# Kernel tuning notes

Hardware: AMD Instinct MI355X
Metric: run time of the kernel (lower is better)

The kernel has to match this reference:

```python
import jax, jax.numpy as jnp
from jax import lax
import numpy as np

TAG_NAMES = ["O", "B-MAT", "I-MAT", "B-PRO", "I-PRO", "B-APL", "I-APL", "B-SMT", "I-SMT", "B-CMT", "I-CMT", "B-DSC", "I-DSC"]
IMP = -100.0


def _init_crf_params(key):
    # torchcrf initializes uniform(-0.1, 0.1); CRF_NEW then clamps invalid
    # BIO transitions to -100 per define_invalid_crf_transitions/init_crf_transitions.
    K = len(TAG_NAMES)
    k1, k2, k3 = jax.random.split(key, 3)
    start = np.array(jax.random.uniform(k1, (K,), minval=-0.1, maxval=0.1), dtype=np.float32)
    end = np.array(jax.random.uniform(k2, (K,), minval=-0.1, maxval=0.1), dtype=np.float32)
    trans = np.array(jax.random.uniform(k3, (K, K), minval=-0.1, maxval=0.1), dtype=np.float32)
    pref = [t[0] for t in TAG_NAMES]
    ent = [t.split('-')[1] if '-' in t else '' for t in TAG_NAMES]
    for i in range(K):
        if pref[i] in ('B', 'I'):  # invalid begin/end for BIO
            start[i] = IMP
            end[i] = IMP
    for i in range(K):
        for j in range(K):
            # invalid_transitions_position: O -> I  (B->P, I->P are empty sets)
            if pref[i] == 'O' and pref[j] == 'I':
                trans[i, j] = IMP
            # invalid_transitions_tags: B->I, I->I across different entity types
            if pref[i] in ('B', 'I') and pref[j] == 'I' and ent[i] != ent[j]:
                trans[i, j] = IMP
    return jnp.asarray(start), jnp.asarray(end), jnp.asarray(trans)


def setup_inputs() -> dict:
    key = jax.random.key(0)
    k_em, k_tag, k_p = jax.random.split(key, 3)
    B, T, K = 4096, 512, len(TAG_NAMES)
    emissions = jax.random.normal(k_em, (B, T, K), dtype=jnp.float32)
    tags = jax.random.randint(k_tag, (B, T), 0, K, dtype=jnp.int64)
    mask = jnp.ones((B, T), dtype=bool)
    start_transitions, end_transitions, transitions = _init_crf_params(k_p)
    return {"emissions": emissions, "tags": tags, "mask": mask,
            "start_transitions": start_transitions,
            "end_transitions": end_transitions,
            "transitions": transitions}


def reference(emissions, tags, mask, start_transitions, end_transitions, transitions):
    # torchcrf CRF.forward with batch_first=True, reduction='sum':
    # returns sum over batch of log p(tags | emissions).
    B, T, K = emissions.shape
    maskf = mask.astype(emissions.dtype)

    # ---- numerator: score of the given tag path ----
    emit = jnp.take_along_axis(emissions, tags[..., None], axis=2)[..., 0]  # [B,T]
    trans = transitions[tags[:, :-1], tags[:, 1:]]                           # [B,T-1]
    num = start_transitions[tags[:, 0]] + emit[:, 0]
    num = num + jnp.sum((trans + emit[:, 1:]) * maskf[:, 1:], axis=1)
    seq_ends = jnp.sum(mask.astype(jnp.int32), axis=1) - 1                   # [B]
    last_tags = tags[jnp.arange(B), seq_ends]
    num = num + end_transitions[last_tags]

    # ---- denominator: log partition via forward-algorithm scan over time ----
    em_t = jnp.swapaxes(emissions, 0, 1)   # [T,B,K]
    mask_t = jnp.swapaxes(mask, 0, 1)      # [T,B]
    score0 = start_transitions + em_t[0]   # [B,K]

    def step(score, xs):
        em, m = xs  # em: [B,K], m: [B]
        # broadcast: [B,K_from,1] + [K_from,K_to] + [B,1,K_to]
        nxt = jax.nn.logsumexp(score[:, :, None] + transitions[None] + em[:, None, :], axis=1)
        return jnp.where(m[:, None], nxt, score), None

    score, _ = lax.scan(step, score0, (em_t[1:], mask_t[1:]))
    denom = jax.nn.logsumexp(score + end_transitions, axis=1)  # [B]

    return jnp.sum(num - denom)
```

## Files before the change

kernel.cpp:

```cpp
#include <hip/hip_runtime.h>


typedef float f4 __attribute__((ext_vector_type(4)));
typedef short s4 __attribute__((ext_vector_type(4)));
typedef int   i2 __attribute__((ext_vector_type(2)));

#define AS1 __attribute__((address_space(1)))
#define AS3 __attribute__((address_space(3)))
typedef unsigned int u32;

__device__ __forceinline__ unsigned pack_bf16(float x, float y) {
  return __builtin_amdgcn_perm(__float_as_uint(y) + 0x8000u,
                               __float_as_uint(x) + 0x8000u, 0x07060302u);
}
__device__ __forceinline__ void dma4(const float* g, float* l) {
  __builtin_amdgcn_global_load_lds((const AS1 u32*)g, (AS3 u32*)l, 4, 0, 0);
}
#define WAITV18 asm volatile("s_waitcnt vmcnt(18)" ::: "memory")
#define WAITV0  asm volatile("s_waitcnt vmcnt(0)"  ::: "memory")
#define LGKM0   asm volatile("s_waitcnt lgkmcnt(0)" ::: "memory")

__global__ void __launch_bounds__(128, 1)
crf_main(const float* __restrict__ em,
         const int*   __restrict__ tags,
         const float* __restrict__ startT,
         const float* __restrict__ endT,
         const float* __restrict__ trans,
         float* __restrict__ partial)
{
  __shared__ __align__(16) float emBuf[2][2][1088];
  __shared__ __align__(16) int   tgBuf[2][2][64];
  __shared__ float ldsT[256], ldsS[16], ldsE[16];
  __shared__ float pFa[8][16];
  __shared__ float lsF[8], numF[8], resB[8];
  __shared__ int   tag255s[8];

  const int tid = threadIdx.x;
  for (int i = tid; i < 169; i += 128) {
    const int r = i / 13, c = i - r * 13;
    ldsT[r * 16 + c] = trans[i];
  }
  if (tid < 13) ldsS[tid] = startT[tid];
  if (tid >= 16 && tid < 29) ldsE[tid - 16] = endT[tid - 16];
  __syncthreads();

  const int lane = tid & 63;
  const int n    = lane & 15;
  const int n8   = n & 7;
  const int q    = lane >> 4;
  const int wid  = tid >> 6;
  const bool is_fwd = (wid == 0);

  int emOff[17];
#pragma unroll
  for (int d = 0; d < 17; ++d) {
    const int wd = d * 64 + lane;
    const int s  = wd / 136;
    const int rem = wd - s * 136;
    int tt = rem >> 4; if (tt > 7) tt = 7;
    int st = rem & 15; if (st > 12) st = 12;
    emOff[d] = (blockIdx.x * 8 + s) * 6656 + tt * 13 + st;
  }
  const int tgOff = (blockIdx.x * 8 + (lane >> 3)) * 512 + (lane & 7);

  s4 afrag;
  {
    float av[4];
#pragma unroll
    for (int i = 0; i < 4; ++i) {
      const int kk = 4 * q + i;
      av[i] = (kk < 13 && n < 13)
            ? __expf(is_fwd ? ldsT[kk * 16 + n] : ldsT[n * 16 + kk]) : 0.0f;
    }
    i2 ai = { (int)pack_bf16(av[0], av[1]), (int)pack_bf16(av[2], av[3]) };
    afrag = __builtin_bit_cast(s4, ai);
  }
  f4 D;
#pragma unroll
  for (int r = 0; r < 4; ++r) {
    const int m = 4 * q + r;
    D[r] = (m < 13) ? __expf(is_fwd ? ldsS[m] : ldsE[m]) : 0.0f;
  }

  float* bufE0 = emBuf[wid][0]; float* bufE1 = emBuf[wid][1];
  int*   bufT0 = tgBuf[wid][0]; int*   bufT1 = tgBuf[wid][1];
  const int off = (q < 3) ? 4 * q : 12;

  float logscale = 0, em_acc = 0, trans_acc = 0, start_t0 = 0;
  int tg_hi = 0, tg_lo = 0, tg511 = 0;
  f4 emA[8], emB[8];
  int4 tqA[2], tqB[2];
  float sDs0 = 0, sDs1 = 0, sDs2 = 0, sDs3 = 0;

#define ISSUE(RB, BE, BT) do {                                         \
    const float* _er = em + (size_t)(RB) * 13;                         \
    _Pragma("unroll")                                                  \
    for (int d_ = 0; d_ < 17; ++d_) dma4(_er + emOff[d_], (BE) + 64 * d_); \
    dma4((const float*)(tags + (RB) + tgOff), (float*)(BT));           \
  } while (0)

#define READC(BE, BT, ER, TQ) do {                                     \
    _Pragma("unroll")                                                  \
    for (int t_ = 0; t_ < 8; ++t_)                                     \
      ER[t_] = *(const f4*)&(BE)[n8 * 136 + t_ * 16 + off];            \
    TQ[0] = *(const int4*)&(BT)[n8 * 8];                               \
    TQ[1] = *(const int4*)&(BT)[n8 * 8 + 4];                           \
  } while (0)

#define TG8(TQ, k) ((k) < 4 ? ((k)==0?TQ[0].x:(k)==1?TQ[0].y:(k)==2?TQ[0].z:TQ[0].w) \
                            : ((k)==4?TQ[1].x:(k)==5?TQ[1].y:(k)==6?TQ[1].z:TQ[1].w))

#define RENORM4() do {                                                 \
    float cm_ = fmaxf(fmaxf(Ds0, Ds1), fmaxf(Ds2, Ds3));               \
    cm_ = fmaxf(cm_, __shfl_xor(cm_, 16, 64));                         \
    cm_ = fmaxf(cm_, __shfl_xor(cm_, 32, 64));                         \
    const float rc_ = __builtin_amdgcn_rcpf(cm_);                      \
    Ds0 *= rc_; Ds1 *= rc_; Ds2 *= rc_; Ds3 *= rc_;                    \
    logscale += __logf(cm_);                                           \
  } while (0)

#define CORE(EM4, RN, TG, SAVE) do {                                   \
    const f4 _e4 = (EM4);                                              \
    const float e0 = __expf(_e4.x), e1 = __expf(_e4.y),                \
                e2 = __expf(_e4.z), e3 = __expf(_e4.w);                \
    float Ds0 = D[0]*e0, Ds1 = D[1]*e1, Ds2 = D[2]*e2, Ds3 = D[3]*e3;  \
    if (RN) RENORM4();                                                 \
    { const int dd = (TG) - 4 * q;                                     \
      const float v01 = (dd & 1) ? _e4.y : _e4.x;                      \
      const float v23 = (dd & 1) ? _e4.w : _e4.z;                      \
      const float vv  = (dd & 2) ? v23 : v01;                          \
      em_acc += ((unsigned)dd <= 3u) ? vv : 0.0f; }                    \
    if (SAVE) { sDs0 = Ds0; sDs1 = Ds1; sDs2 = Ds2; sDs3 = Ds3; }      \
    { i2 bi_ = { (int)pack_bf16(Ds0, Ds1), (int)pack_bf16(Ds2, Ds3) }; \
      D = __builtin_amdgcn_mfma_f32_16x16x16bf16_1k(                   \
              afrag, __builtin_bit_cast(s4, bi_),                      \
              (f4){0.f, 0.f, 0.f, 0.f}, 0, 0, 0); }                    \
  } while (0)

#define BKF(TQ, C) do {                                                \
    if ((C) == 0) start_t0 = ldsS[TG8(TQ, 0)];                         \
    else trans_acc += ldsT[tg_hi * 16 + TG8(TQ, 0)];                   \
    _Pragma("unroll")                                                  \
    for (int k_ = 1; k_ < 8; ++k_)                                     \
      trans_acc += ldsT[TG8(TQ, k_ - 1) * 16 + TG8(TQ, k_)];           \
    tg_hi = TG8(TQ, 7);                                                \
  } while (0)

#define BKB(TQ, C) do {                                                \
    if ((C) == 0) tg511 = TG8(TQ, 7);                                  \
    else trans_acc += ldsT[TG8(TQ, 7) * 16 + tg_lo];                   \
    _Pragma("unroll")                                                  \
    for (int k_ = 0; k_ < 7; ++k_)                                     \
      trans_acc += ldsT[TG8(TQ, k_) * 16 + TG8(TQ, k_ + 1)];           \
    tg_lo = TG8(TQ, 0);                                                \
  } while (0)

#define COMPF(ER, TQ, C) do {                                          \
    _Pragma("unroll")                                                  \
    for (int k_ = 0; k_ < 8; ++k_)                                     \
      CORE(ER[k_], (k_ == 7), TG8(TQ, k_), ((C) == 31 && k_ == 7));    \
  } while (0)

#define COMPB(ER, TQ) do {                                             \
    _Pragma("unroll")                                                  \
    for (int kk_ = 0; kk_ < 8; ++kk_) {                                \
      const int k_ = 7 - kk_;                                          \
      CORE(ER[k_], (kk_ == 7), TG8(TQ, k_), false);                    \
    }                                                                  \
  } while (0)

  if (is_fwd) {
    ISSUE(0, bufE0, bufT0);
    ISSUE(8, bufE1, bufT1);
    WAITV18;
    READC(bufE0, bufT0, emA, tqA);
    for (int c = 0; c < 32; c += 2) {
      LGKM0;
      if (c < 30) { ISSUE(8 * (c + 2), bufE0, bufT0); WAITV18; } else WAITV0;
      BKF(tqA, c);
      READC(bufE1, bufT1, emB, tqB);
      COMPF(emA, tqA, c);
      LGKM0;
      if (c < 29) { ISSUE(8 * (c + 3), bufE1, bufT1); WAITV18; } else WAITV0;
      BKF(tqB, c + 1);
      if (c < 30) READC(bufE0, bufT0, emA, tqA);
      COMPF(emB, tqB, c + 1);
    }
    float emr = em_acc + __shfl_xor(em_acc, 16, 64);
    emr += __shfl_xor(emr, 32, 64);
    if (n < 8) {
      *(f4*)&pFa[n8][4 * q] = (f4){sDs0, sDs1, sDs2, sDs3};
      if (q == 0) {
        lsF[n8] = logscale;
        numF[n8] = start_t0 + emr + trans_acc;
        tag255s[n8] = tg_hi;
      }
    }
    __syncthreads();
    __syncthreads();
  } else {
    ISSUE(504, bufE0, bufT0);
    ISSUE(496, bufE1, bufT1);
    WAITV18;
    READC(bufE0, bufT0, emA, tqA);
    for (int c = 0; c < 32; c += 2) {
      LGKM0;
      if (c < 30) { ISSUE(504 - 8 * (c + 2), bufE0, bufT0); WAITV18; } else WAITV0;
      BKB(tqA, c);
      READC(bufE1, bufT1, emB, tqB);
      COMPB(emA, tqA);
      LGKM0;
      if (c < 29) { ISSUE(504 - 8 * (c + 3), bufE1, bufT1); WAITV18; } else WAITV0;
      BKB(tqB, c + 1);
      if (c < 30) READC(bufE0, bufT0, emA, tqA);
      COMPB(emB, tqB);
    }
    __syncthreads();
    const f4 al = *(const f4*)&pFa[n8][4 * q];
    float z = al.x * D[0] + al.y * D[1] + al.z * D[2] + al.w * D[3];
    z += __shfl_xor(z, 16, 64);
    z += __shfl_xor(z, 32, 64);
    float emr = em_acc + __shfl_xor(em_acc, 16, 64);
    emr += __shfl_xor(emr, 32, 64);
    const float denom = lsF[n8] + logscale + __logf(z);
    const float num   = numF[n8] + emr + trans_acc
                      + ldsT[tag255s[n8] * 16 + tg_lo]
                      + ldsE[tg511];
    if (q == 0 && n < 8) resB[n8] = num - denom;
    __syncthreads();
  }
  if (tid == 0) {
    float s = 0.0f;
#pragma unroll
    for (int i = 0; i < 8; ++i) s += resB[i];
    partial[blockIdx.x] = s;
  }

#undef ISSUE
#undef READC
#undef TG8
#undef RENORM4
#undef CORE
#undef BKF
#undef BKB
#undef COMPF
#undef COMPB
}

__global__ void __launch_bounds__(256)
crf_reduce(const float* __restrict__ part, float* __restrict__ out, int n)
{
  float v = 0.0f;
  for (int i = threadIdx.x; i < n; i += 256) v += part[i];
#pragma unroll
  for (int o = 32; o > 0; o >>= 1) v += __shfl_down(v, o);
  __shared__ float w[4];
  if ((threadIdx.x & 63) == 0) w[threadIdx.x >> 6] = v;
  __syncthreads();
  if (threadIdx.x == 0) out[0] = (w[0] + w[1]) + (w[2] + w[3]);
}

extern "C" void kernel_launch(void* const* d_in, const int* in_sizes, int n_in,
                              void* d_out, int out_size, void* d_ws, size_t ws_size,
                              hipStream_t stream) {
  const float* em   = (const float*)d_in[0];
  const int*   tags = (const int*)d_in[1];
  const float* st   = (const float*)d_in[3];
  const float* en   = (const float*)d_in[4];
  const float* tr   = (const float*)d_in[5];
  float* part = (float*)d_ws;

  crf_main<<<512, 128, 0, stream>>>(em, tags, st, en, tr, part);
  crf_reduce<<<1, 256, 0, stream>>>(part, (float*)d_out, 512);
}
```

Measured before the change: 207.1 us.

## Use 16-byte LDS DMA loads with four-deep staging ring buffer

Replaces the 17 per-lane 4-byte global-to-LDS DMA loads per chunk with 4 contiguous 16-byte DMA loads plus one for tags, keeping the raw row layout in LDS. The double buffer becomes a 4-slot ring so loads are issued four chunks ahead, with adjusted vmcnt waits. LDS reads now gather unaligned scalars at stride 13 instead of aligned f4 loads, which may add LDS bank conflicts and instruction count. Past the end of the sequence the loop issues dummy loads to keep the wait counts consistent.

```diff
diff --git a/kernel.cpp b/kernel.cpp
--- a/kernel.cpp
+++ b/kernel.cpp
@@ -13,10 +13,11 @@
   return __builtin_amdgcn_perm(__float_as_uint(y) + 0x8000u,
                                __float_as_uint(x) + 0x8000u, 0x07060302u);
 }
-__device__ __forceinline__ void dma4(const float* g, float* l) {
-  __builtin_amdgcn_global_load_lds((const AS1 u32*)g, (AS3 u32*)l, 4, 0, 0);
-}
-#define WAITV18 asm volatile("s_waitcnt vmcnt(18)" ::: "memory")
+__device__ __forceinline__ void dma16(const void* g, void* l) {
+  __builtin_amdgcn_global_load_lds((const AS1 u32*)g, (AS3 u32*)l, 16, 0, 0);
+}
+#define WAITV15 asm volatile("s_waitcnt vmcnt(15)" ::: "memory")
+#define WAITV10 asm volatile("s_waitcnt vmcnt(10)" ::: "memory")
 #define WAITV0  asm volatile("s_waitcnt vmcnt(0)"  ::: "memory")
 #define LGKM0   asm volatile("s_waitcnt lgkmcnt(0)" ::: "memory")
 
@@ -28,8 +29,7 @@
          const float* __restrict__ trans,
          float* __restrict__ partial)
 {
-  __shared__ __align__(16) float emBuf[2][2][1088];
-  __shared__ __align__(16) int   tgBuf[2][2][64];
+  __shared__ __align__(16) char stage[2][4][5120];
   __shared__ float ldsT[256], ldsS[16], ldsE[16];
   __shared__ float pFa[8][16];
   __shared__ float lsF[8], numF[8], resB[8];
@@ -50,18 +50,21 @@
   const int q    = lane >> 4;
   const int wid  = tid >> 6;
   const bool is_fwd = (wid == 0);
-
-  int emOff[17];
-#pragma unroll
-  for (int d = 0; d < 17; ++d) {
-    const int wd = d * 64 + lane;
-    const int s  = wd / 136;
-    const int rem = wd - s * 136;
-    int tt = rem >> 4; if (tt > 7) tt = 7;
-    int st = rem & 15; if (st > 12) st = 12;
-    emOff[d] = (blockIdx.x * 8 + s) * 6656 + tt * 13 + st;
-  }
-  const int tgOff = (blockIdx.x * 8 + (lane >> 3)) * 512 + (lane & 7);
+  const int seqBase = blockIdx.x * 8;
+  const char* emB8 = (const char*)em   + (size_t)seqBase * 26624;
+  const char* tgB8 = (const char*)tags + (size_t)seqBase * 2048;
+
+  int emOffB[4];
+#pragma unroll
+  for (int d = 0; d < 4; ++d) {
+    int o = d * 1024 + lane * 16;
+    if (o >= 3328) o = (lane & 15) * 16;
+    const int s = o / 416;
+    emOffB[d] = s * 26624 + (o - s * 416);
+  }
+  int tgo = lane * 16;
+  if (tgo >= 256) tgo = (lane & 15) * 16;
+  const int tgOffB = (tgo >> 5) * 2048 + (tgo & 31);
 
   s4 afrag;
   {
@@ -82,29 +85,34 @@
     D[r] = (m < 13) ? __expf(is_fwd ? ldsS[m] : ldsE[m]) : 0.0f;
   }
 
-  float* bufE0 = emBuf[wid][0]; float* bufE1 = emBuf[wid][1];
-  int*   bufT0 = tgBuf[wid][0]; int*   bufT1 = tgBuf[wid][1];
-  const int off = (q < 3) ? 4 * q : 12;
-
+  const int stq = (q < 3) ? 4 * q : 12;
   float logscale = 0, em_acc = 0, trans_acc = 0, start_t0 = 0;
   int tg_hi = 0, tg_lo = 0, tg511 = 0;
   f4 emA[8], emB[8];
   int4 tqA[2], tqB[2];
   float sDs0 = 0, sDs1 = 0, sDs2 = 0, sDs3 = 0;
 
-#define ISSUE(RB, BE, BT) do {                                         \
-    const float* _er = em + (size_t)(RB) * 13;                         \
-    _Pragma("unroll")                                                  \
-    for (int d_ = 0; d_ < 17; ++d_) dma4(_er + emOff[d_], (BE) + 64 * d_); \
-    dma4((const float*)(tags + (RB) + tgOff), (float*)(BT));           \
-  } while (0)
-
-#define READC(BE, BT, ER, TQ) do {                                     \
-    _Pragma("unroll")                                                  \
-    for (int t_ = 0; t_ < 8; ++t_)                                     \
-      ER[t_] = *(const f4*)&(BE)[n8 * 136 + t_ * 16 + off];            \
-    TQ[0] = *(const int4*)&(BT)[n8 * 8];                               \
-    TQ[1] = *(const int4*)&(BT)[n8 * 8 + 4];                           \
+#define ISSUE(T0, BUF) do {                                            \
+    const char* _eb = emB8 + (size_t)(T0) * 52;                        \
+    char* _lb = stage[wid][BUF];                                       \
+    dma16(_eb + emOffB[0], _lb);                                       \
+    dma16(_eb + emOffB[1], _lb + 1024);                                \
+    dma16(_eb + emOffB[2], _lb + 2048);                                \
+    dma16(_eb + emOffB[3], _lb + 3072);                                \
+    dma16(tgB8 + (size_t)(T0) * 4 + tgOffB, _lb + 4096);               \
+  } while (0)
+
+#define READC(BUF, ER, TQ) do {                                        \
+    const float* _el = (const float*)stage[wid][BUF];                  \
+    const int _b0 = n8 * 104 + stq;                                    \
+    _Pragma("unroll")                                                  \
+    for (int k_ = 0; k_ < 8; ++k_) {                                   \
+      const int _w = _b0 + k_ * 13;                                    \
+      ER[k_] = (f4){_el[_w], _el[_w + 1], _el[_w + 2], _el[_w + 3]};   \
+    }                                                                  \
+    const int* _tl = (const int*)(stage[wid][BUF] + 4096);             \
+    TQ[0] = *(const int4*)&_tl[n8 * 8];                                \
+    TQ[1] = *(const int4*)&_tl[n8 * 8 + 4];                            \
   } while (0)
 
 #define TG8(TQ, k) ((k) < 4 ? ((k)==0?TQ[0].x:(k)==1?TQ[0].y:(k)==2?TQ[0].z:TQ[0].w) \
@@ -170,22 +178,25 @@
   } while (0)
 
   if (is_fwd) {
-    ISSUE(0, bufE0, bufT0);
-    ISSUE(8, bufE1, bufT1);
-    WAITV18;
-    READC(bufE0, bufT0, emA, tqA);
+    ISSUE(0, 0); ISSUE(8, 1); ISSUE(16, 2); ISSUE(24, 3);
+    WAITV15;
+    READC(0, emA, tqA);
+    LGKM0;
     for (int c = 0; c < 32; c += 2) {
-      LGKM0;
-      if (c < 30) { ISSUE(8 * (c + 2), bufE0, bufT0); WAITV18; } else WAITV0;
+      WAITV10;
+      READC((c + 1) & 3, emB, tqB);
       BKF(tqA, c);
-      READC(bufE1, bufT1, emB, tqB);
       COMPF(emA, tqA, c);
       LGKM0;
-      if (c < 29) { ISSUE(8 * (c + 3), bufE1, bufT1); WAITV18; } else WAITV0;
+      { const int cc = c + 4; ISSUE(cc <= 31 ? 8 * cc : 248, c & 3); }
+      WAITV10;
+      if (c < 30) READC((c + 2) & 3, emA, tqA);
       BKF(tqB, c + 1);
-      if (c < 30) READC(bufE0, bufT0, emA, tqA);
       COMPF(emB, tqB, c + 1);
-    }
+      LGKM0;
+      { const int cc = c + 5; ISSUE(cc <= 31 ? 8 * cc : 248, (c + 1) & 3); }
+    }
+    WAITV0;
     float emr = em_acc + __shfl_xor(em_acc, 16, 64);
     emr += __shfl_xor(emr, 32, 64);
     if (n < 8) {
@@ -199,22 +210,25 @@
     __syncthreads();
     __syncthreads();
   } else {
-    ISSUE(504, bufE0, bufT0);
-    ISSUE(496, bufE1, bufT1);
-    WAITV18;
-    READC(bufE0, bufT0, emA, tqA);
+    ISSUE(504, 0); ISSUE(496, 1); ISSUE(488, 2); ISSUE(480, 3);
+    WAITV15;
+    READC(0, emA, tqA);
+    LGKM0;
     for (int c = 0; c < 32; c += 2) {
-      LGKM0;
-      if (c < 30) { ISSUE(504 - 8 * (c + 2), bufE0, bufT0); WAITV18; } else WAITV0;
+      WAITV10;
+      READC((c + 1) & 3, emB, tqB);
       BKB(tqA, c);
-      READC(bufE1, bufT1, emB, tqB);
       COMPB(emA, tqA);
       LGKM0;
-      if (c < 29) { ISSUE(504 - 8 * (c + 3), bufE1, bufT1); WAITV18; } else WAITV0;
+      { const int cc = c + 4; ISSUE(cc <= 31 ? 504 - 8 * cc : 256, c & 3); }
+      WAITV10;
+      if (c < 30) READC((c + 2) & 3, emA, tqA);
       BKB(tqB, c + 1);
-      if (c < 30) READC(bufE0, bufT0, emA, tqA);
       COMPB(emB, tqB);
-    }
+      LGKM0;
+      { const int cc = c + 5; ISSUE(cc <= 31 ? 504 - 8 * cc : 256, (c + 1) & 3); }
+    }
+    WAITV0;
     __syncthreads();
     const f4 al = *(const f4*)&pFa[n8][4 * q];
     float z = al.x * D[0] + al.y * D[1] + al.z * D[2] + al.w * D[3];
```

Result: faster. 194.4 us (-6.1%).
